# Optimization experiments

Hardware: AMD Instinct MI355X
Metric: run time of the kernel (lower is better)

The kernel has to match this reference:

```python
import jax, jax.numpy as jnp
import numpy as np

NUM_MIRNA = 20000
NUM_GENE = 30000
N = NUM_MIRNA + NUM_GENE  # 50000 homogeneous nodes
R = 4                      # num_relations
E = 1000000                # num edges
IN_C, HID, OUT, NB = 128, 128, 64, 10


def setup_inputs() -> dict:
    key = jax.random.key(0)
    ks = jax.random.split(key, 20)
    s = 0.05
    inp = {}
    inp["x_mirna"] = jax.random.normal(ks[0], (NUM_MIRNA, 256), jnp.float32)
    inp["x_gene"] = jax.random.normal(ks[1], (NUM_GENE, 512), jnp.float32)
    inp["edge_index"] = jax.random.randint(ks[2], (2, E), 0, N)
    inp["edge_type"] = jax.random.randint(ks[3], (E,), 0, R)
    # per-node-type input projections
    inp["lin_w_m"] = jax.random.normal(ks[4], (256, IN_C), jnp.float32) * s
    inp["lin_b_m"] = jnp.zeros((IN_C,), jnp.float32)
    inp["lin_w_g"] = jax.random.normal(ks[5], (512, IN_C), jnp.float32) * s
    inp["lin_b_g"] = jnp.zeros((IN_C,), jnp.float32)
    # RGCNConv layer 1 (basis decomposition)
    inp["comp1"] = jax.random.normal(ks[6], (R, NB), jnp.float32) * s
    inp["basis1"] = jax.random.normal(ks[7], (NB, IN_C, HID), jnp.float32) * s
    inp["root1"] = jax.random.normal(ks[8], (IN_C, HID), jnp.float32) * s
    inp["bias1"] = jnp.zeros((HID,), jnp.float32)
    # RGCNConv layer 2
    inp["comp2"] = jax.random.normal(ks[9], (R, NB), jnp.float32) * s
    inp["basis2"] = jax.random.normal(ks[10], (NB, HID, OUT), jnp.float32) * s
    inp["root2"] = jax.random.normal(ks[11], (HID, OUT), jnp.float32) * s
    inp["bias2"] = jnp.zeros((OUT,), jnp.float32)
    return inp


def rgcn_conv(x, src, dst, etype, comp, basis, root, bias):
    # W_r = sum_b comp[r,b] * basis[b] : [R, I, O]
    W = jnp.einsum('rb,bio->rio', comp, basis)
    # transform every node under every relation: [R, N, O]
    h = jnp.einsum('ni,rio->rno', x, W)
    # gather per-edge message from (relation, source) pair: [E, O]
    msg = h[etype, src]
    # per-(relation, dst) mean aggregation (PyG RGCNConv aggr='mean')
    seg = etype * N + dst
    summed = jax.ops.segment_sum(msg, seg, num_segments=R * N)
    cnt = jax.ops.segment_sum(jnp.ones((msg.shape[0],), msg.dtype), seg,
                              num_segments=R * N)
    mean = summed / jnp.maximum(cnt, 1.0)[:, None]
    agg = mean.reshape(R, N, -1).sum(0)  # sum over relations
    return agg + x @ root + bias


def reference(x_mirna, x_gene, edge_index, edge_type,
              lin_w_m, lin_b_m, lin_w_g, lin_b_g,
              comp1, basis1, root1, bias1,
              comp2, basis2, root2, bias2):
    xm = x_mirna @ lin_w_m + lin_b_m
    xg = x_gene @ lin_w_g + lin_b_g
    x = jnp.concatenate([xm, xg], axis=0)  # to_homogeneous, miRNA first
    src, dst = edge_index[0], edge_index[1]
    x = rgcn_conv(x, src, dst, edge_type, comp1, basis1, root1, bias1)
    x = rgcn_conv(x, src, dst, edge_type, comp2, basis2, root2, bias2)
    return x[:NUM_MIRNA], x[NUM_MIRNA:]
```

## Files before the change

### kernel.cpp

```cpp
#include <hip/hip_runtime.h>
#include <hip/hip_bf16.h>

#define NUM_MIRNA 20000
#define NUM_GENE  30000
#define NN        50000
#define RR        4
#define EE        1000000
#define IN_C      128
#define HIDC      128
#define OUTC      64
#define NBASIS    10
#define NSEG      (RR * NN)
#define NSEGP     200704
#define KFUSE     640
#define SROW      512

#define NBKT   256
#define BSH    8
#define NBKTU  ((NN + 255) >> 8)
#define CHUNK  4096
#define NCHUNK ((EE + CHUNK - 1) / CHUNK)

typedef __attribute__((ext_vector_type(8))) short bf16x8;
typedef __attribute__((ext_vector_type(4))) float f32x4;
typedef __attribute__((ext_vector_type(2))) float f32x2;

__device__ inline ushort f2bf(float x) {
    uint u = __float_as_uint(x);
    uint r = u + 0x7fffu + ((u >> 16) & 1u);
    return (ushort)(r >> 16);
}
__device__ inline uint pack2bf(float lo, float hi) {
    return (uint)f2bf(lo) | ((uint)f2bf(hi) << 16);
}
__device__ inline f32x2 up2(uint u) {
    return (f32x2){__uint_as_float(u << 16), __uint_as_float(u & 0xffff0000u)};
}

#define GLOAD_LDS16(gsrc, ldst)                                                \
    __builtin_amdgcn_global_load_lds(                                          \
        (const __attribute__((address_space(1))) void*)(gsrc),                 \
        (__attribute__((address_space(3))) void*)(ldst), 16, 0, 0)

__global__ void prep_k(const float* __restrict__ lin_w_m, const float* __restrict__ lin_w_g,
                       const float* __restrict__ comp1, const float* __restrict__ basis1,
                       const float* __restrict__ root1,
                       const float* __restrict__ comp2, const float* __restrict__ basis2,
                       const float* __restrict__ root2,
                       ushort* __restrict__ Wtm, ushort* __restrict__ Wtg,
                       ushort* __restrict__ Wt1s, ushort* __restrict__ Wt2s) {
    int gidx = blockIdx.x * 256 + threadIdx.x;
    if (gidx < 32768) {
        int idx = gidx;
        int o = idx >> 8, k = idx & 255;
        Wtm[idx] = f2bf(lin_w_m[(size_t)k * IN_C + o]);
    } else if (gidx < 98304) {
        int idx = gidx - 32768;
        int o = idx >> 9, k = idx & 511;
        Wtg[idx] = f2bf(lin_w_g[(size_t)k * IN_C + o]);
    } else if (gidx < 180224) {
        int idx = gidx - 98304;
        int o = idx / KFUSE, k = idx % KFUSE;
        float acc;
        if (k < 512) {
            int r = k >> 7, i = k & 127;
            acc = 0.f;
#pragma unroll
            for (int b = 0; b < NBASIS; ++b)
                acc += comp1[r * NBASIS + b] * basis1[((size_t)b * 128 + i) * HIDC + o];
        } else {
            acc = root1[(size_t)(k - 512) * HIDC + o];
        }
        Wt1s[idx] = f2bf(acc);
    } else if (gidx < 221184) {
        int idx = gidx - 180224;
        int o = idx / KFUSE, k = idx % KFUSE;
        float acc;
        if (k < 512) {
            int r = k >> 7, i = k & 127;
            acc = 0.f;
#pragma unroll
            for (int b = 0; b < NBASIS; ++b)
                acc += comp2[r * NBASIS + b] * basis2[((size_t)b * 128 + i) * OUTC + o];
        } else {
            acc = root2[(size_t)(k - 512) * OUTC + o];
        }
        Wt2s[idx] = f2bf(acc);
    }
}

template <int NT, int K, bool OUT_BF16, bool ROOTX, bool A_F32>
__global__ __launch_bounds__(256) void sgemm_k(
    const void* __restrict__ Av, const ushort* __restrict__ xroot,
    const ushort* __restrict__ Wt, const float* __restrict__ bias,
    void* __restrict__ Cout, int M)
{
    constexpr int OC = 2 * NT * 16;
    constexpr int BK = 64;
    constexpr int NTILE = K / BK;
    constexpr int AS = ROOTX ? SROW : K;
    const ushort* A  = (const ushort*)Av;
    const float*  Af = (const float*)Av;

    __shared__ __align__(16) ushort As[2 * 4096];

    const int tid  = threadIdx.x;
    const int lane = tid & 63;
    const int wid  = tid >> 6;
    const int wm   = wid >> 1;
    const int wn   = wid & 1;
    const int l15  = lane & 15;
    const int lg   = lane >> 4;
    const int rowBase = blockIdx.x * 64;
    const int colBase = wn * NT * 16;

    f32x4 acc[2][NT];
#pragma unroll
    for (int mt = 0; mt < 2; ++mt)
#pragma unroll
        for (int nt = 0; nt < NT; ++nt)
            acc[mt][nt] = (f32x4){0.f, 0.f, 0.f, 0.f};

    float4 fA[2][2];

    auto STAGE = [&](int buf, int t) {
        const int kc = t * BK;
#pragma unroll
        for (int i = 0; i < 2; ++i) {
            int L   = i * 4096 + tid * 16;
            int row = L >> 7;
            int bs  = (L & 127) ^ ((row & 7) << 4);
            int grow = rowBase + row; if (grow >= M) grow = M - 1;
            const ushort* src;
            if (!ROOTX || kc < SROW)
                src = A + (size_t)grow * AS + kc + (bs >> 1);
            else
                src = xroot + (size_t)grow * IN_C + (kc - SROW) + (bs >> 1);
            GLOAD_LDS16(src, &As[(size_t)buf * 4096 + (L >> 1)]);
        }
    };
    auto STAGE_LOAD = [&](int t) {
        const int kc = t * BK;
#pragma unroll
        for (int i = 0; i < 2; ++i) {
            int L   = i * 4096 + tid * 16;
            int row = L >> 7;
            int bs  = (L & 127) ^ ((row & 7) << 4);
            int grow = rowBase + row; if (grow >= M) grow = M - 1;
            const float* src = Af + (size_t)grow * K + kc + (bs >> 1);
            fA[i][0] = *(const float4*)src;
            fA[i][1] = *(const float4*)(src + 4);
        }
    };
    auto STAGE_WRITE = [&](int buf) {
#pragma unroll
        for (int i = 0; i < 2; ++i) {
            int L = i * 4096 + tid * 16;
            float4 f0 = fA[i][0], f1 = fA[i][1];
            bf16x8 tv;
            tv[0] = (short)f2bf(f0.x); tv[1] = (short)f2bf(f0.y);
            tv[2] = (short)f2bf(f0.z); tv[3] = (short)f2bf(f0.w);
            tv[4] = (short)f2bf(f1.x); tv[5] = (short)f2bf(f1.y);
            tv[6] = (short)f2bf(f1.z); tv[7] = (short)f2bf(f1.w);
            *(bf16x8*)&As[(size_t)buf * 4096 + (L >> 1)] = tv;
        }
    };

    if (A_F32) { STAGE_LOAD(0); STAGE_WRITE(0); }
    else       STAGE(0, 0);
    __syncthreads();

#pragma unroll
    for (int t = 0; t < NTILE; ++t) {
        const int kc  = t * BK;
        const int buf = t & 1;

        bf16x8 bB[2][NT];
#pragma unroll
        for (int kk = 0; kk < 2; ++kk)
#pragma unroll
            for (int nt = 0; nt < NT; ++nt)
                bB[kk][nt] = *(const bf16x8*)(
                    Wt + (size_t)(colBase + nt * 16 + l15) * K + kc + kk * 32 + lg * 8);

        if (t + 1 < NTILE) {
            if (A_F32) STAGE_LOAD(t + 1);
            else       STAGE(buf ^ 1, t + 1);
        }

        bf16x8 aF[2][2];
#pragma unroll
        for (int mt = 0; mt < 2; ++mt)
#pragma unroll
            for (int kk = 0; kk < 2; ++kk) {
                int row = wm * 32 + mt * 16 + l15;
                int kb  = kk * 64 + lg * 16;
                aF[mt][kk] = *(const bf16x8*)&As[
                    (size_t)buf * 4096 + row * 64 + ((kb ^ ((row & 7) << 4)) >> 1)];
            }

#pragma unroll
        for (int kk = 0; kk < 2; ++kk)
#pragma unroll
            for (int nt = 0; nt < NT; ++nt)
#pragma unroll
                for (int mt = 0; mt < 2; ++mt)
                    acc[mt][nt] = __builtin_amdgcn_mfma_f32_16x16x32_bf16(
                        aF[mt][kk], bB[kk][nt], acc[mt][nt], 0, 0, 0);

        if (A_F32 && t + 1 < NTILE) STAGE_WRITE(buf ^ 1);
        __syncthreads();
    }

#pragma unroll
    for (int nt = 0; nt < NT; ++nt) {
        int n = colBase + nt * 16 + l15;
        float bv = bias ? bias[n] : 0.f;
#pragma unroll
        for (int mt = 0; mt < 2; ++mt) {
#pragma unroll
            for (int q = 0; q < 4; ++q) {
                int m = rowBase + wm * 32 + mt * 16 + lg * 4 + q;
                if (m < M) {
                    float v = acc[mt][nt][q] + bv;
                    size_t off = (size_t)m * OC + n;
                    if (OUT_BF16) ((ushort*)Cout)[off] = f2bf(v);
                    else          ((float*)Cout)[off]  = v;
                }
            }
        }
    }
}

__global__ __launch_bounds__(256) void bs0_k(const int* __restrict__ dstA,
                                             int* __restrict__ bcnt) {
    __shared__ int h[NBKT];
    int t = threadIdx.x;
    h[t] = 0;
    __syncthreads();
    int e0 = blockIdx.x * CHUNK;
    int n = EE - e0; if (n > CHUNK) n = CHUNK;
    for (int i = t; i < n; i += 256)
        atomicAdd(&h[dstA[e0 + i] >> BSH], 1);
    __syncthreads();
    if (h[t]) atomicAdd(&bcnt[t], h[t]);
}

__global__ void bscan_k(const int* __restrict__ bcnt, int* __restrict__ bbase,
                        int* __restrict__ bcur) {
    __shared__ int sm[NBKT];
    int t = threadIdx.x;
    int v = bcnt[t];
    sm[t] = v; __syncthreads();
    for (int off = 1; off < NBKT; off <<= 1) {
        int x = (t >= off) ? sm[t - off] : 0;
        __syncthreads();
        sm[t] += x;
        __syncthreads();
    }
    int ex = sm[t] - v;
    bbase[t] = ex;
    bcur[t]  = ex;
}

__global__ __launch_bounds__(256) void bs1_k(const int* __restrict__ srcA,
                                             const int* __restrict__ dstA,
                                             const int* __restrict__ et,
                                             int* __restrict__ bcur,
                                             uint* __restrict__ bpay) {
    __shared__ int h[NBKT], cur[NBKT], boff[NBKT];
    __shared__ uint lpay[CHUNK];
    __shared__ unsigned char lbkt[CHUNK];
    int t = threadIdx.x;
    h[t] = 0; cur[t] = 0;
    __syncthreads();
    int e0 = blockIdx.x * CHUNK;
    int n = EE - e0; if (n > CHUNK) n = CHUNK;
    for (int i = t; i < n; i += 256) {
        int e = e0 + i;
        int d = dstA[e];
        int s2 = d * 4 + et[e];
        int b = d >> BSH;
        lpay[i] = ((uint)(s2 & 1023) << 17) | (uint)srcA[e];
        lbkt[i] = (unsigned char)b;
        atomicAdd(&h[b], 1);
    }
    __syncthreads();
    if (h[t]) boff[t] = atomicAdd(&bcur[t], h[t]);
    __syncthreads();
    for (int i = t; i < n; i += 256) {
        int b = lbkt[i];
        int slot = atomicAdd(&cur[b], 1);
        bpay[boff[b] + slot] = lpay[i];
    }
}

__global__ __launch_bounds__(256) void sortbkt_k(
    const uint* __restrict__ bpay, const int* __restrict__ bbase,
    const int* __restrict__ bcnt, int* __restrict__ sorted,
    int* __restrict__ cnt, int* __restrict__ base, float* __restrict__ inv)
{
    __shared__ int hist[1024];
    __shared__ int tsum[256];
    const int b = blockIdx.x;
    const int t = threadIdx.x;
    const int segbase = b << 10;

#pragma unroll
    for (int i = 0; i < 4; ++i) hist[t + i * 256] = 0;
    __syncthreads();

    const int e0 = bbase[b];
    const int n  = bcnt[b];
    for (int i = t; i < n; i += 256)
        atomicAdd(&hist[(int)(bpay[e0 + i] >> 17)], 1);
    __syncthreads();

    int h0 = hist[t * 4], h1 = hist[t * 4 + 1], h2 = hist[t * 4 + 2], h3 = hist[t * 4 + 3];
    int s = h0 + h1 + h2 + h3;
    tsum[t] = s; __syncthreads();
    for (int off = 1; off < 256; off <<= 1) {
        int x = (t >= off) ? tsum[t - off] : 0;
        __syncthreads();
        tsum[t] += x;
        __syncthreads();
    }
    int run = (t > 0) ? tsum[t - 1] : 0;
    int b0 = run, b1 = run + h0, b2 = b1 + h1, b3 = b2 + h2;

    ((int4*)cnt)[(segbase >> 2) + t]  = make_int4(h0, h1, h2, h3);
    ((int4*)base)[(segbase >> 2) + t] = make_int4(e0 + b0, e0 + b1, e0 + b2, e0 + b3);
    ((float4*)inv)[(segbase >> 2) + t] = make_float4(
        1.0f / fmaxf((float)h0, 1.0f), 1.0f / fmaxf((float)h1, 1.0f),
        1.0f / fmaxf((float)h2, 1.0f), 1.0f / fmaxf((float)h3, 1.0f));

    hist[t * 4] = b0; hist[t * 4 + 1] = b1; hist[t * 4 + 2] = b2; hist[t * 4 + 3] = b3;
    __syncthreads();

    for (int i = t; i < n; i += 256) {
        uint val = bpay[e0 + i];
        int pos = atomicAdd(&hist[(int)(val >> 17)], 1);
        sorted[e0 + pos] = (int)((val & 0x1FFFFu) << 8);
    }
}

__global__ __launch_bounds__(256) void gatherS_k(
    const ushort* __restrict__ x, const int* __restrict__ sorted,
    const int* __restrict__ base, const int* __restrict__ cnt,
    const float* __restrict__ inv, ushort* __restrict__ S)
{
    int d = (blockIdx.x * 256 + threadIdx.x) >> 6;
    int lane = threadIdx.x & 63;
    if (d >= NN) return;
    const char* xb = (const char*)x;
    uint4* Sp = (uint4*)S;
    const int slot = lane >> 4;
    const int cg   = lane & 15;
    const int cgb  = cg << 4;

    int4   b4 = ((const int4*)base)[d];
    int4   c4 = ((const int4*)cnt)[d];
    float4 w4 = ((const float4*)inv)[d];
    const int ofr[4]  = {0, b4.y - b4.x, b4.z - b4.x, b4.w - b4.x};
    const int cnts[4] = {c4.x, c4.y, c4.z, c4.w};
    const float wts[4] = {w4.x, w4.y, w4.z, w4.w};
    const int tot = (b4.w + c4.w) - b4.x;

    f32x2 acc[4][4];
#pragma unroll
    for (int r = 0; r < 4; ++r)
#pragma unroll
        for (int t = 0; t < 4; ++t) acc[r][t] = (f32x2){0.f, 0.f};

    if (tot <= 64) {
        int idx = sorted[b4.x + lane];
        int maxn = max(max(cnts[0], cnts[1]), max(cnts[2], cnts[3]));
        for (int j = 0; j < maxn; j += 4) {
            int e = j + slot;
#pragma unroll
            for (int r = 0; r < 4; ++r) {
                int off = __shfl(idx, ofr[r] + e);
                if (e < cnts[r]) {
                    uint4 v = *(const uint4*)(xb + off + cgb);
                    acc[r][0] += up2(v.x);
                    acc[r][1] += up2(v.y);
                    acc[r][2] += up2(v.z);
                    acc[r][3] += up2(v.w);
                }
            }
        }
    } else {
#pragma unroll
        for (int r = 0; r < 4; ++r) {
            int s0 = b4.x + ofr[r];
            int s1 = s0 + cnts[r];
            for (int i0 = s0; i0 < s1; i0 += 64) {
                int idx2 = sorted[i0 + lane];
                int n2 = s1 - i0; if (n2 > 64) n2 = 64;
                for (int j = 0; j < n2; j += 4) {
                    int e = j + slot;
                    int off = __shfl(idx2, e);
                    if (e < n2) {
                        uint4 v = *(const uint4*)(xb + off + cgb);
                        acc[r][0] += up2(v.x);
                        acc[r][1] += up2(v.y);
                        acc[r][2] += up2(v.z);
                        acc[r][3] += up2(v.w);
                    }
                }
            }
        }
    }

#pragma unroll
    for (int r = 0; r < 4; ++r) {
        float wt = wts[r];
#pragma unroll
        for (int t = 0; t < 4; ++t) {
            acc[r][t].x += __shfl_xor(acc[r][t].x, 16);
            acc[r][t].y += __shfl_xor(acc[r][t].y, 16);
            acc[r][t].x += __shfl_xor(acc[r][t].x, 32);
            acc[r][t].y += __shfl_xor(acc[r][t].y, 32);
        }
        if (slot == 0) {
            uint4 o;
            o.x = pack2bf(acc[r][0].x * wt, acc[r][0].y * wt);
            o.y = pack2bf(acc[r][1].x * wt, acc[r][1].y * wt);
            o.z = pack2bf(acc[r][2].x * wt, acc[r][2].y * wt);
            o.w = pack2bf(acc[r][3].x * wt, acc[r][3].y * wt);
            Sp[(size_t)d * 64 + r * 16 + cg] = o;
        }
    }
}

extern "C" void kernel_launch(void* const* d_in, const int* in_sizes, int n_in,
                              void* d_out, int out_size, void* d_ws, size_t ws_size,
                              hipStream_t stream) {
    const float* x_mirna = (const float*)d_in[0];
    const float* x_gene  = (const float*)d_in[1];
    const int*   eidx    = (const int*)d_in[2];
    const int*   etype   = (const int*)d_in[3];
    const float* lin_w_m = (const float*)d_in[4];
    const float* lin_b_m = (const float*)d_in[5];
    const float* lin_w_g = (const float*)d_in[6];
    const float* lin_b_g = (const float*)d_in[7];
    const float* comp1   = (const float*)d_in[8];
    const float* basis1  = (const float*)d_in[9];
    const float* root1   = (const float*)d_in[10];
    const float* bias1   = (const float*)d_in[11];
    const float* comp2   = (const float*)d_in[12];
    const float* basis2  = (const float*)d_in[13];
    const float* root2   = (const float*)d_in[14];
    const float* bias2   = (const float*)d_in[15];

    const int* srcA = eidx;
    const int* dstA = eidx + EE;

    char* p = (char*)d_ws;
    ushort* x0bf = (ushort*)p; p += (size_t)(NN + 1) * IN_C * 2;
    ushort* x1bf = (ushort*)p; p += (size_t)(NN + 1) * HIDC * 2;
    ushort* S    = (ushort*)p; p += (size_t)NN * SROW * 2;
    ushort* Wtm  = (ushort*)p; p += (size_t)IN_C * 256 * 2;
    ushort* Wtg  = (ushort*)p; p += (size_t)IN_C * 512 * 2;
    ushort* Wt1s = (ushort*)p; p += (size_t)HIDC * KFUSE * 2;
    ushort* Wt2s = (ushort*)p; p += (size_t)OUTC * KFUSE * 2;
    float* inv   = (float*)p;  p += (size_t)NSEGP * 4;
    int* cnt     = (int*)p;    p += (size_t)NSEGP * 4;
    int* base    = (int*)p;    p += (size_t)NSEGP * 4;
    int* bcnt    = (int*)p;    p += NBKT * 4;
    int* bbase   = (int*)p;    p += NBKT * 4;
    int* bcur    = (int*)p;    p += NBKT * 4;
    int* sorted  = (int*)p;    p += (size_t)(EE + 64) * 4;
    uint* bpay   = (uint*)p;   p += (size_t)EE * 4;

    float* outp = (float*)d_out;

    hipMemsetAsync(bcnt, 0, NBKT * sizeof(int), stream);

    prep_k<<<(221184 + 255) / 256, 256, 0, stream>>>(
        lin_w_m, lin_w_g, comp1, basis1, root1, comp2, basis2, root2,
        Wtm, Wtg, Wt1s, Wt2s);

    bs0_k<<<NCHUNK, 256, 0, stream>>>(dstA, bcnt);
    bscan_k<<<1, NBKT, 0, stream>>>(bcnt, bbase, bcur);
    bs1_k<<<NCHUNK, 256, 0, stream>>>(srcA, dstA, etype, bcur, bpay);
    sortbkt_k<<<NBKTU, 256, 0, stream>>>(bpay, bbase, bcnt, sorted, cnt, base, inv);

    sgemm_k<4, 256, true, false, true><<<dim3((NUM_MIRNA + 63) / 64), 256, 0, stream>>>(
        x_mirna, nullptr, Wtm, lin_b_m, x0bf, NUM_MIRNA);
    sgemm_k<4, 512, true, false, true><<<dim3((NUM_GENE + 63) / 64), 256, 0, stream>>>(
        x_gene, nullptr, Wtg, lin_b_g, x0bf + (size_t)NUM_MIRNA * IN_C, NUM_GENE);

    gatherS_k<<<(NN * 64 + 255) / 256, 256, 0, stream>>>(x0bf, sorted, base, cnt, inv, S);
    sgemm_k<4, KFUSE, true, true, false><<<dim3((NN + 63) / 64), 256, 0, stream>>>(
        S, x0bf, Wt1s, bias1, x1bf, NN);

    gatherS_k<<<(NN * 64 + 255) / 256, 256, 0, stream>>>(x1bf, sorted, base, cnt, inv, S);
    sgemm_k<2, KFUSE, false, true, false><<<dim3((NN + 63) / 64), 256, 0, stream>>>(
        S, x1bf, Wt2s, bias2, outp, NN);
}
```

Baseline: 265.8 us.

## Merge independent preprocessing kernels into combined launches to overlap work

Combines the weight-prep kernel with the destination bucket histogram into one launch, and the bucket scatter with the two input-projection GEMMs into another, dispatching by block index. This cuts launch count and lets the independent sort and GEMM work run concurrently instead of back to back. The cost is that the merged kernel uses the largest shared-memory footprint of its branches (about 23 KB) for every block, which may reduce occupancy for the GEMM blocks. Smaller register pressure mixing is also possible.

Result: faster. 254.0 us (-4.4%).

```diff
diff --git a/kernel.cpp b/kernel.cpp
--- a/kernel.cpp
+++ b/kernel.cpp
@@ -20,6 +20,10 @@
 #define NBKTU  ((NN + 255) >> 8)
 #define CHUNK  4096
 #define NCHUNK ((EE + CHUNK - 1) / CHUNK)
+#define PREPN  221184
+#define PREPB  ((PREPN + 255) / 256)
+#define PMB    ((NUM_MIRNA + 63) / 64)
+#define PGB    ((NUM_GENE + 63) / 64)
 
 typedef __attribute__((ext_vector_type(8))) short bf16x8;
 typedef __attribute__((ext_vector_type(4))) float f32x4;
@@ -42,14 +46,11 @@
         (const __attribute__((address_space(1))) void*)(gsrc),                 \
         (__attribute__((address_space(3))) void*)(ldst), 16, 0, 0)
 
-__global__ void prep_k(const float* __restrict__ lin_w_m, const float* __restrict__ lin_w_g,
-                       const float* __restrict__ comp1, const float* __restrict__ basis1,
-                       const float* __restrict__ root1,
-                       const float* __restrict__ comp2, const float* __restrict__ basis2,
-                       const float* __restrict__ root2,
-                       ushort* __restrict__ Wtm, ushort* __restrict__ Wtg,
-                       ushort* __restrict__ Wt1s, ushort* __restrict__ Wt2s) {
-    int gidx = blockIdx.x * 256 + threadIdx.x;
+__device__ void dev_prep(int gidx,
+                         const float* lin_w_m, const float* lin_w_g,
+                         const float* comp1, const float* basis1, const float* root1,
+                         const float* comp2, const float* basis2, const float* root2,
+                         ushort* Wtm, ushort* Wtg, ushort* Wt1s, ushort* Wt2s) {
     if (gidx < 32768) {
         int idx = gidx;
         int o = idx >> 8, k = idx & 255;
@@ -72,7 +73,7 @@
             acc = root1[(size_t)(k - 512) * HIDC + o];
         }
         Wt1s[idx] = f2bf(acc);
-    } else if (gidx < 221184) {
+    } else if (gidx < PREPN) {
         int idx = gidx - 180224;
         int o = idx / KFUSE, k = idx % KFUSE;
         float acc;
@@ -89,11 +90,91 @@
     }
 }
 
+__device__ void dev_bs0(int blk, const int* dstA, int* bcnt, char* smem) {
+    int* h = (int*)smem;
+    int t = threadIdx.x;
+    h[t] = 0;
+    __syncthreads();
+    int e0 = blk * CHUNK;
+    int n = EE - e0; if (n > CHUNK) n = CHUNK;
+    for (int i = t; i < n; i += 256)
+        atomicAdd(&h[dstA[e0 + i] >> BSH], 1);
+    __syncthreads();
+    if (h[t]) atomicAdd(&bcnt[t], h[t]);
+}
+
+__global__ __launch_bounds__(256) void init_k(
+    const int* __restrict__ dstA, int* __restrict__ bcnt,
+    const float* __restrict__ lin_w_m, const float* __restrict__ lin_w_g,
+    const float* __restrict__ comp1, const float* __restrict__ basis1,
+    const float* __restrict__ root1,
+    const float* __restrict__ comp2, const float* __restrict__ basis2,
+    const float* __restrict__ root2,
+    ushort* __restrict__ Wtm, ushort* __restrict__ Wtg,
+    ushort* __restrict__ Wt1s, ushort* __restrict__ Wt2s) {
+    __shared__ __align__(16) char smem[1024];
+    int b = blockIdx.x;
+    if (b < NCHUNK) {
+        dev_bs0(b, dstA, bcnt, smem);
+    } else {
+        int gidx = (b - NCHUNK) * 256 + threadIdx.x;
+        dev_prep(gidx, lin_w_m, lin_w_g, comp1, basis1, root1,
+                 comp2, basis2, root2, Wtm, Wtg, Wt1s, Wt2s);
+    }
+}
+
+__global__ void bscan_k(const int* __restrict__ bcnt, int* __restrict__ bbase,
+                        int* __restrict__ bcur) {
+    __shared__ int sm[NBKT];
+    int t = threadIdx.x;
+    int v = bcnt[t];
+    sm[t] = v; __syncthreads();
+    for (int off = 1; off < NBKT; off <<= 1) {
+        int x = (t >= off) ? sm[t - off] : 0;
+        __syncthreads();
+        sm[t] += x;
+        __syncthreads();
+    }
+    int ex = sm[t] - v;
+    bbase[t] = ex;
+    bcur[t]  = ex;
+}
+
+__device__ void dev_bs1(int blk, const int* srcA, const int* dstA, const int* et,
+                        int* bcur, uint* bpay, char* smem) {
+    int* h    = (int*)smem;
+    int* cur  = h + NBKT;
+    int* boff = cur + NBKT;
+    uint* lpay = (uint*)(boff + NBKT);
+    unsigned char* lbkt = (unsigned char*)(lpay + CHUNK);
+    int t = threadIdx.x;
+    h[t] = 0; cur[t] = 0;
+    __syncthreads();
+    int e0 = blk * CHUNK;
+    int n = EE - e0; if (n > CHUNK) n = CHUNK;
+    for (int i = t; i < n; i += 256) {
+        int e = e0 + i;
+        int d = dstA[e];
+        int s2 = d * 4 + et[e];
+        int b = d >> BSH;
+        lpay[i] = ((uint)(s2 & 1023) << 17) | (uint)srcA[e];
+        lbkt[i] = (unsigned char)b;
+        atomicAdd(&h[b], 1);
+    }
+    __syncthreads();
+    if (h[t]) boff[t] = atomicAdd(&bcur[t], h[t]);
+    __syncthreads();
+    for (int i = t; i < n; i += 256) {
+        int b = lbkt[i];
+        int slot = atomicAdd(&cur[b], 1);
+        bpay[boff[b] + slot] = lpay[i];
+    }
+}
+
 template <int NT, int K, bool OUT_BF16, bool ROOTX, bool A_F32>
-__global__ __launch_bounds__(256) void sgemm_k(
-    const void* __restrict__ Av, const ushort* __restrict__ xroot,
-    const ushort* __restrict__ Wt, const float* __restrict__ bias,
-    void* __restrict__ Cout, int M)
+__device__ void dev_sgemm(const void* Av, const ushort* xroot,
+                          const ushort* Wt, const float* bias,
+                          void* Cout, int M, int blk, char* smem)
 {
     constexpr int OC = 2 * NT * 16;
     constexpr int BK = 64;
@@ -101,8 +182,7 @@
     constexpr int AS = ROOTX ? SROW : K;
     const ushort* A  = (const ushort*)Av;
     const float*  Af = (const float*)Av;
-
-    __shared__ __align__(16) ushort As[2 * 4096];
+    ushort* As = (ushort*)smem;
 
     const int tid  = threadIdx.x;
     const int lane = tid & 63;
@@ -111,7 +191,7 @@
     const int wn   = wid & 1;
     const int l15  = lane & 15;
     const int lg   = lane >> 4;
-    const int rowBase = blockIdx.x * 64;
+    const int rowBase = blk * 64;
     const int colBase = wn * NT * 16;
 
     f32x4 acc[2][NT];
@@ -232,66 +312,37 @@
     }
 }
 
-__global__ __launch_bounds__(256) void bs0_k(const int* __restrict__ dstA,
-                                             int* __restrict__ bcnt) {
-    __shared__ int h[NBKT];
-    int t = threadIdx.x;
-    h[t] = 0;
-    __syncthreads();
-    int e0 = blockIdx.x * CHUNK;
-    int n = EE - e0; if (n > CHUNK) n = CHUNK;
-    for (int i = t; i < n; i += 256)
-        atomicAdd(&h[dstA[e0 + i] >> BSH], 1);
-    __syncthreads();
-    if (h[t]) atomicAdd(&bcnt[t], h[t]);
-}
-
-__global__ void bscan_k(const int* __restrict__ bcnt, int* __restrict__ bbase,
-                        int* __restrict__ bcur) {
-    __shared__ int sm[NBKT];
-    int t = threadIdx.x;
-    int v = bcnt[t];
-    sm[t] = v; __syncthreads();
-    for (int off = 1; off < NBKT; off <<= 1) {
-        int x = (t >= off) ? sm[t - off] : 0;
-        __syncthreads();
-        sm[t] += x;
-        __syncthreads();
-    }
-    int ex = sm[t] - v;
-    bbase[t] = ex;
-    bcur[t]  = ex;
-}
-
-__global__ __launch_bounds__(256) void bs1_k(const int* __restrict__ srcA,
-                                             const int* __restrict__ dstA,
-                                             const int* __restrict__ et,
-                                             int* __restrict__ bcur,
-                                             uint* __restrict__ bpay) {
-    __shared__ int h[NBKT], cur[NBKT], boff[NBKT];
-    __shared__ uint lpay[CHUNK];
-    __shared__ unsigned char lbkt[CHUNK];
-    int t = threadIdx.x;
-    h[t] = 0; cur[t] = 0;
-    __syncthreads();
-    int e0 = blockIdx.x * CHUNK;
-    int n = EE - e0; if (n > CHUNK) n = CHUNK;
-    for (int i = t; i < n; i += 256) {
-        int e = e0 + i;
-        int d = dstA[e];
-        int s2 = d * 4 + et[e];
-        int b = d >> BSH;
-        lpay[i] = ((uint)(s2 & 1023) << 17) | (uint)srcA[e];
-        lbkt[i] = (unsigned char)b;
-        atomicAdd(&h[b], 1);
-    }
-    __syncthreads();
-    if (h[t]) boff[t] = atomicAdd(&bcur[t], h[t]);
-    __syncthreads();
-    for (int i = t; i < n; i += 256) {
-        int b = lbkt[i];
-        int slot = atomicAdd(&cur[b], 1);
-        bpay[boff[b] + slot] = lpay[i];
+template <int NT, int K, bool OUT_BF16, bool ROOTX, bool A_F32>
+__global__ __launch_bounds__(256) void sgemm_k(
+    const void* __restrict__ Av, const ushort* __restrict__ xroot,
+    const ushort* __restrict__ Wt, const float* __restrict__ bias,
+    void* __restrict__ Cout, int M)
+{
+    __shared__ __align__(16) char smem[16384];
+    dev_sgemm<NT, K, OUT_BF16, ROOTX, A_F32>(Av, xroot, Wt, bias, Cout, M,
+                                             blockIdx.x, smem);
+}
+
+__global__ __launch_bounds__(256) void work_k(
+    const int* __restrict__ srcA, const int* __restrict__ dstA,
+    const int* __restrict__ etype, int* __restrict__ bcur,
+    uint* __restrict__ bpay,
+    const float* __restrict__ x_mirna, const float* __restrict__ x_gene,
+    const ushort* __restrict__ Wtm, const ushort* __restrict__ Wtg,
+    const float* __restrict__ lin_b_m, const float* __restrict__ lin_b_g,
+    ushort* __restrict__ x0bf)
+{
+    __shared__ __align__(16) char smem[23552];
+    int b = blockIdx.x;
+    if (b < NCHUNK) {
+        dev_bs1(b, srcA, dstA, etype, bcur, bpay, smem);
+    } else if (b < NCHUNK + PMB) {
+        dev_sgemm<4, 256, true, false, true>(
+            x_mirna, nullptr, Wtm, lin_b_m, x0bf, NUM_MIRNA, b - NCHUNK, smem);
+    } else {
+        dev_sgemm<4, 512, true, false, true>(
+            x_gene, nullptr, Wtg, lin_b_g, x0bf + (size_t)NUM_MIRNA * IN_C,
+            NUM_GENE, b - NCHUNK - PMB, smem);
     }
 }
 
@@ -477,19 +528,17 @@
 
     hipMemsetAsync(bcnt, 0, NBKT * sizeof(int), stream);
 
-    prep_k<<<(221184 + 255) / 256, 256, 0, stream>>>(
-        lin_w_m, lin_w_g, comp1, basis1, root1, comp2, basis2, root2,
-        Wtm, Wtg, Wt1s, Wt2s);
-
-    bs0_k<<<NCHUNK, 256, 0, stream>>>(dstA, bcnt);
+    init_k<<<NCHUNK + PREPB, 256, 0, stream>>>(
+        dstA, bcnt, lin_w_m, lin_w_g, comp1, basis1, root1,
+        comp2, basis2, root2, Wtm, Wtg, Wt1s, Wt2s);
+
     bscan_k<<<1, NBKT, 0, stream>>>(bcnt, bbase, bcur);
-    bs1_k<<<NCHUNK, 256, 0, stream>>>(srcA, dstA, etype, bcur, bpay);
+
+    work_k<<<NCHUNK + PMB + PGB, 256, 0, stream>>>(
+        srcA, dstA, etype, bcur, bpay, x_mirna, x_gene,
+        Wtm, Wtg, lin_b_m, lin_b_g, x0bf);
+
     sortbkt_k<<<NBKTU, 256, 0, stream>>>(bpay, bbase, bcnt, sorted, cnt, base, inv);
-
-    sgemm_k<4, 256, true, false, true><<<dim3((NUM_MIRNA + 63) / 64), 256, 0, stream>>>(
-        x_mirna, nullptr, Wtm, lin_b_m, x0bf, NUM_MIRNA);
-    sgemm_k<4, 512, true, false, true><<<dim3((NUM_GENE + 63) / 64), 256, 0, stream>>>(
-        x_gene, nullptr, Wtg, lin_b_g, x0bf + (size_t)NUM_MIRNA * IN_C, NUM_GENE);
 
     gatherS_k<<<(NN * 64 + 255) / 256, 256, 0, stream>>>(x0bf, sorted, base, cnt, inv, S);
     sgemm_k<4, KFUSE, true, true, false><<<dim3((NN + 63) / 64), 256, 0, stream>>>(
```
